# Kernel optimization log

Hardware: AMD Instinct MI355X
Metric: run time of the kernel (lower is better)

## Reference

```python
import jax, jax.numpy as jnp
import numpy as np

B, N, K, D = 4, 8192, 16, 128
G = D // 4  # spatial-encoding groups, 4 feature channels each ('a4')
BN_EPS = 1e-5


def setup_inputs() -> dict:
    key = jax.random.key(0)
    ks = jax.random.split(key, 8)
    x = jax.random.normal(ks[0], (B, N, D), jnp.float32)
    xyz = jax.random.uniform(ks[1], (B, N, 3), jnp.float32)
    knn = jax.random.randint(ks[2], (B, N, K), 0, N)
    proj_w = jax.random.normal(ks[3], (D, D), jnp.float32) * 0.02  # nn.Linear(in,out,bias=False) weight [out,in]
    coor = jax.random.normal(ks[4], (G * 3,), jnp.float32) * 0.5   # init_coor(out_dim//4).flatten()
    scale = jnp.full((G,), 0.1, jnp.float32)                        # zeros + 0.1
    bn_weight = jnp.ones((D,), jnp.float32)                          # init=1.0
    bn_bias = jnp.zeros((D,), jnp.float32)
    return dict(x=x, xyz=xyz, knn=knn, proj_w=proj_w, coor=coor,
                scale=scale, bn_weight=bn_weight, bn_bias=bn_bias)


def reference(x, xyz, knn, proj_w, coor, scale, bn_weight, bn_bias):
    Bb, Nn, _ = x.shape
    # 1) linear projection (no bias)
    h = jnp.einsum('bnc,dc->bnd', x, proj_w)  # [B,N,D]
    # 2) learned spatial position encoding weights: (4, G) = [cx,cy,cz,scale^2]
    w = jnp.concatenate([coor.reshape(-1, 3).T, (scale * scale)[None, :]], axis=0)
    # 3) KNN gathers
    bidx = jnp.arange(Bb)[:, None, None]
    xyz_n = xyz[bidx, knn]                      # [B,N,K,3]
    rel = xyz_n - xyz[:, :, None, :]            # relative coords
    f4 = jnp.concatenate([rel, jnp.sum(rel * rel, axis=-1, keepdims=True)], axis=-1)  # [B,N,K,4]
    e = jnp.einsum('bnkf,fg->bnkg', f4, w)      # [B,N,K,G] encoding per group
    hn = h[bidx, knn]                           # [B,N,K,D] neighbor features
    # 4) add encoding per group of 4 channels, max-aggregate over K neighbors
    g = hn.reshape(Bb, Nn, K, G, 4) + e[..., None]
    agg = jnp.max(g, axis=2).reshape(Bb, Nn, D)
    # 5) BatchNorm1d over B*N rows (training-mode batch stats, biased var)
    flat = agg.reshape(-1, D)
    mean = jnp.mean(flat, axis=0)
    var = jnp.mean(jnp.square(flat - mean), axis=0)
    y = (flat - mean) * jax.lax.rsqrt(var + BN_EPS) * bn_weight + bn_bias
    return y.reshape(Bb, Nn, D)
```

## Files before the change

### kernel.cpp

```cpp
#include <hip/hip_runtime.h>
#include <math.h>

#define BB 4
#define NN 8192
#define KK 16
#define DD 128
#define GG 32
#define NPTS (BB * NN)
#define GATHER_BLOCKS 2048
#define BN_EPS 1e-5f

__global__ void transpose_w(const float* __restrict__ w, float* __restrict__ wt) {
    int i = blockIdx.x * 256 + threadIdx.x;
    int d = i >> 7;
    int c = i & 127;
    wt[c * 128 + d] = w[d * 128 + c];
}

__global__ __launch_bounds__(256) void gemm_h(const float* __restrict__ x,
                                              const float* __restrict__ wt,
                                              float* __restrict__ h) {
    __shared__ float xs[64][128];
    const int block_row = blockIdx.x * 64;
    const int t = threadIdx.x;

    const float4* xg = reinterpret_cast<const float4*>(x + (size_t)block_row * 128);
    float4* xs4 = reinterpret_cast<float4*>(&xs[0][0]);
#pragma unroll
    for (int i = 0; i < 8; ++i) xs4[t + 256 * i] = xg[t + 256 * i];
    __syncthreads();

    const int ty = t >> 5;
    const int tx = t & 31;
    const int r0 = ty * 8;
    const int c0 = tx * 4;

    float acc[8][4];
#pragma unroll
    for (int r = 0; r < 8; ++r)
#pragma unroll
        for (int j = 0; j < 4; ++j) acc[r][j] = 0.f;

    for (int c4 = 0; c4 < 32; ++c4) {
        float4 wv[4];
#pragma unroll
        for (int j = 0; j < 4; ++j)
            wv[j] = *reinterpret_cast<const float4*>(wt + (size_t)(c4 * 4 + j) * 128 + c0);
#pragma unroll
        for (int r = 0; r < 8; ++r) {
            float4 xv = *reinterpret_cast<const float4*>(&xs[r0 + r][c4 * 4]);
            const float xc[4] = {xv.x, xv.y, xv.z, xv.w};
#pragma unroll
            for (int j = 0; j < 4; ++j) {
                acc[r][0] = fmaf(xc[j], wv[j].x, acc[r][0]);
                acc[r][1] = fmaf(xc[j], wv[j].y, acc[r][1]);
                acc[r][2] = fmaf(xc[j], wv[j].z, acc[r][2]);
                acc[r][3] = fmaf(xc[j], wv[j].w, acc[r][3]);
            }
        }
    }

#pragma unroll
    for (int r = 0; r < 8; ++r) {
        float4 o = make_float4(acc[r][0], acc[r][1], acc[r][2], acc[r][3]);
        *reinterpret_cast<float4*>(h + (size_t)(block_row + r0 + r) * 128 + c0) = o;
    }
}

__global__ __launch_bounds__(256) void gather_max(const float* __restrict__ h,
                                                  const float* __restrict__ xyz,
                                                  const int* __restrict__ knn,
                                                  const float* __restrict__ coor,
                                                  const float* __restrict__ scale,
                                                  float* __restrict__ out,
                                                  float* __restrict__ partials) {
    const int t = threadIdx.x;
    const int g = t & 31;
    const int sub = t >> 5;

    const float c0w = coor[g * 3 + 0];
    const float c1w = coor[g * 3 + 1];
    const float c2w = coor[g * 3 + 2];
    const float sg = scale[g];
    const float s2 = sg * sg;

    float lsum[4] = {0.f, 0.f, 0.f, 0.f};
    float lsq[4]  = {0.f, 0.f, 0.f, 0.f};

#pragma unroll
    for (int it = 0; it < 2; ++it) {
        const int p = blockIdx.x * 16 + it * 8 + sub;
        const int b = p >> 13;
        const float* ctr = xyz + (size_t)p * 3;
        const float cx = ctr[0], cy = ctr[1], cz = ctr[2];
        const int* kn = knn + (size_t)p * KK;

        float4 acc = make_float4(-INFINITY, -INFINITY, -INFINITY, -INFINITY);

#pragma unroll
        for (int k = 0; k < KK; ++k) {
            const int idx = kn[k];
            const int row = b * NN + idx;
            const float* nb = xyz + (size_t)row * 3;
            const float rx = nb[0] - cx;
            const float ry = nb[1] - cy;
            const float rz = nb[2] - cz;
            const float r2 = rx * rx + ry * ry + rz * rz;
            const float e = rx * c0w + ry * c1w + rz * c2w + r2 * s2;
            const float4 hv = *reinterpret_cast<const float4*>(h + (size_t)row * 128 + g * 4);
            acc.x = fmaxf(acc.x, hv.x + e);
            acc.y = fmaxf(acc.y, hv.y + e);
            acc.z = fmaxf(acc.z, hv.z + e);
            acc.w = fmaxf(acc.w, hv.w + e);
        }

        *reinterpret_cast<float4*>(out + (size_t)p * 128 + g * 4) = acc;

        lsum[0] += acc.x; lsum[1] += acc.y; lsum[2] += acc.z; lsum[3] += acc.w;
        lsq[0] += acc.x * acc.x; lsq[1] += acc.y * acc.y;
        lsq[2] += acc.z * acc.z; lsq[3] += acc.w * acc.w;
    }

    __shared__ float red[8][128];
#pragma unroll
    for (int j = 0; j < 4; ++j) red[sub][g * 4 + j] = lsum[j];
    __syncthreads();
    if (t < 128) {
        float s = 0.f;
#pragma unroll
        for (int s8 = 0; s8 < 8; ++s8) s += red[s8][t];
        partials[(size_t)t * GATHER_BLOCKS + blockIdx.x] = s;
    }
    __syncthreads();
#pragma unroll
    for (int j = 0; j < 4; ++j) red[sub][g * 4 + j] = lsq[j];
    __syncthreads();
    if (t < 128) {
        float q = 0.f;
#pragma unroll
        for (int s8 = 0; s8 < 8; ++s8) q += red[s8][t];
        partials[(size_t)(128 + t) * GATHER_BLOCKS + blockIdx.x] = q;
    }
}

__global__ __launch_bounds__(256) void bn_stats(const float* __restrict__ partials,
                                                const float* __restrict__ bnw,
                                                const float* __restrict__ bnb,
                                                float* __restrict__ stats) {
    const int ch = blockIdx.x;
    const int t = threadIdx.x;
    const float* ps = partials + (size_t)ch * GATHER_BLOCKS;
    const float* pq = partials + (size_t)(128 + ch) * GATHER_BLOCKS;
    float s = 0.f, q = 0.f;
    for (int i = t; i < GATHER_BLOCKS; i += 256) { s += ps[i]; q += pq[i]; }
    __shared__ float rs[256], rq[256];
    rs[t] = s; rq[t] = q;
    __syncthreads();
    for (int off = 128; off > 0; off >>= 1) {
        if (t < off) { rs[t] += rs[t + off]; rq[t] += rq[t + off]; }
        __syncthreads();
    }
    if (t == 0) {
        const float inv_n = 1.0f / (float)NPTS;
        const float mean = rs[0] * inv_n;
        const float var = rq[0] * inv_n - mean * mean;
        const float rstd = rsqrtf(var + BN_EPS);
        const float A = rstd * bnw[ch];
        stats[ch] = A;
        stats[128 + ch] = bnb[ch] - mean * A;
    }
}

__global__ __launch_bounds__(256) void bn_apply(float* __restrict__ out,
                                                const float* __restrict__ stats) {
    const int i = blockIdx.x * 256 + threadIdx.x;
    const int ch4 = i & 31;
    float4 v = reinterpret_cast<float4*>(out)[i];
    const float4 A = reinterpret_cast<const float4*>(stats)[ch4];
    const float4 C = reinterpret_cast<const float4*>(stats + 128)[ch4];
    v.x = fmaf(v.x, A.x, C.x);
    v.y = fmaf(v.y, A.y, C.y);
    v.z = fmaf(v.z, A.z, C.z);
    v.w = fmaf(v.w, A.w, C.w);
    reinterpret_cast<float4*>(out)[i] = v;
}

extern "C" void kernel_launch(void* const* d_in, const int* in_sizes, int n_in,
                              void* d_out, int out_size, void* d_ws, size_t ws_size,
                              hipStream_t stream) {
    const float* x      = (const float*)d_in[0];
    const float* xyz    = (const float*)d_in[1];
    const int*   knn    = (const int*)d_in[2];
    const float* proj_w = (const float*)d_in[3];
    const float* coor   = (const float*)d_in[4];
    const float* scale  = (const float*)d_in[5];
    const float* bnw    = (const float*)d_in[6];
    const float* bnb    = (const float*)d_in[7];
    float* out = (float*)d_out;

    char* ws = (char*)d_ws;
    float* h        = (float*)(ws);
    float* wt       = (float*)(ws + (size_t)NPTS * DD * 4);
    float* partials = (float*)(ws + (size_t)NPTS * DD * 4 + 65536);
    float* stats    = (float*)(ws + (size_t)NPTS * DD * 4 + 65536
                               + (size_t)2 * 128 * GATHER_BLOCKS * 4);

    transpose_w<<<64, 256, 0, stream>>>(proj_w, wt);
    gemm_h<<<NPTS / 64, 256, 0, stream>>>(x, wt, h);
    gather_max<<<GATHER_BLOCKS, 256, 0, stream>>>(h, xyz, knn, coor, scale, out, partials);
    bn_stats<<<128, 256, 0, stream>>>(partials, bnw, bnb, stats);
    bn_apply<<<(NPTS * DD / 4) / 256, 256, 0, stream>>>(out, stats);
}
```

Before: 69.50 us.

## Fuse gather-max, BN stats and BN apply into one persistent kernel with grid barriers

Merges the gather/max kernel, the BN statistics reduction and the BN apply pass into a single kernel of 1024 co-resident blocks. Two atomic grid barriers separate the three phases, and each thread keeps its aggregated values in registers so the output is written once, already normalized. This removes two kernel launches and a full read-modify-write of the output tensor. Blocks are also remapped so each XCD works on one batch half, which should improve L2 locality of the neighbor gathers. The cost is a spin-barrier whose correctness depends on all blocks being resident at once, plus an extra memset launch to clear the flags.

```diff
diff --git a/kernel.cpp b/kernel.cpp
--- a/kernel.cpp
+++ b/kernel.cpp
@@ -7,7 +7,8 @@
 #define DD 128
 #define GG 32
 #define NPTS (BB * NN)
-#define GATHER_BLOCKS 2048
+#define FBLOCKS 1024
+#define PTS_PER_BLOCK 32
 #define BN_EPS 1e-5f
 
 __global__ void transpose_w(const float* __restrict__ w, float* __restrict__ wt) {
@@ -67,16 +68,42 @@
     }
 }
 
-__global__ __launch_bounds__(256) void gather_max(const float* __restrict__ h,
-                                                  const float* __restrict__ xyz,
-                                                  const int* __restrict__ knn,
-                                                  const float* __restrict__ coor,
-                                                  const float* __restrict__ scale,
-                                                  float* __restrict__ out,
-                                                  float* __restrict__ partials) {
+__device__ __forceinline__ void grid_barrier(int* cnt, int* gen) {
+    __syncthreads();
+    if (threadIdx.x == 0) {
+        int prev = __hip_atomic_fetch_add(cnt, 1, __ATOMIC_ACQ_REL, __HIP_MEMORY_SCOPE_AGENT);
+        if (prev == FBLOCKS - 1) {
+            __hip_atomic_store(gen, 1, __ATOMIC_RELEASE, __HIP_MEMORY_SCOPE_AGENT);
+        } else {
+            while (__hip_atomic_load(gen, __ATOMIC_RELAXED, __HIP_MEMORY_SCOPE_AGENT) == 0) {
+                __builtin_amdgcn_s_sleep(8);
+            }
+            (void)__hip_atomic_load(gen, __ATOMIC_ACQUIRE, __HIP_MEMORY_SCOPE_AGENT);
+        }
+    }
+    __syncthreads();
+}
+
+__global__ __launch_bounds__(256, 4) void fused_gbn(const float* __restrict__ h,
+                                                    const float* __restrict__ xyz,
+                                                    const int* __restrict__ knn,
+                                                    const float* __restrict__ coor,
+                                                    const float* __restrict__ scale,
+                                                    const float* __restrict__ bnw,
+                                                    const float* __restrict__ bnb,
+                                                    float* __restrict__ out,
+                                                    float* __restrict__ partials,
+                                                    float* __restrict__ stats,
+                                                    int* __restrict__ flags) {
     const int t = threadIdx.x;
     const int g = t & 31;
     const int sub = t >> 5;
+
+    const int xcd = blockIdx.x & 7;
+    const int jj = blockIdx.x >> 3;
+    const int slot = ((xcd & 1) << 7) + jj;
+    const int b = xcd >> 1;
+    const int pbase = (b << 13) + (slot << 5);
 
     const float c0w = coor[g * 3 + 0];
     const float c1w = coor[g * 3 + 1];
@@ -86,11 +113,11 @@
 
     float lsum[4] = {0.f, 0.f, 0.f, 0.f};
     float lsq[4]  = {0.f, 0.f, 0.f, 0.f};
-
-#pragma unroll
-    for (int it = 0; it < 2; ++it) {
-        const int p = blockIdx.x * 16 + it * 8 + sub;
-        const int b = p >> 13;
+    float4 accv[4];
+
+#pragma unroll
+    for (int it = 0; it < 4; ++it) {
+        const int p = pbase + it * 8 + sub;
         const float* ctr = xyz + (size_t)p * 3;
         const float cx = ctr[0], cy = ctr[1], cz = ctr[2];
         const int* kn = knn + (size_t)p * KK;
@@ -100,7 +127,7 @@
 #pragma unroll
         for (int k = 0; k < KK; ++k) {
             const int idx = kn[k];
-            const int row = b * NN + idx;
+            const int row = (b << 13) + idx;
             const float* nb = xyz + (size_t)row * 3;
             const float rx = nb[0] - cx;
             const float ry = nb[1] - cy;
@@ -114,8 +141,7 @@
             acc.w = fmaxf(acc.w, hv.w + e);
         }
 
-        *reinterpret_cast<float4*>(out + (size_t)p * 128 + g * 4) = acc;
-
+        accv[it] = acc;
         lsum[0] += acc.x; lsum[1] += acc.y; lsum[2] += acc.z; lsum[3] += acc.w;
         lsq[0] += acc.x * acc.x; lsq[1] += acc.y * acc.y;
         lsq[2] += acc.z * acc.z; lsq[3] += acc.w * acc.w;
@@ -129,7 +155,7 @@
         float s = 0.f;
 #pragma unroll
         for (int s8 = 0; s8 < 8; ++s8) s += red[s8][t];
-        partials[(size_t)t * GATHER_BLOCKS + blockIdx.x] = s;
+        partials[(size_t)t * FBLOCKS + blockIdx.x] = s;
     }
     __syncthreads();
 #pragma unroll
@@ -139,50 +165,49 @@
         float q = 0.f;
 #pragma unroll
         for (int s8 = 0; s8 < 8; ++s8) q += red[s8][t];
-        partials[(size_t)(128 + t) * GATHER_BLOCKS + blockIdx.x] = q;
-    }
-}
-
-__global__ __launch_bounds__(256) void bn_stats(const float* __restrict__ partials,
-                                                const float* __restrict__ bnw,
-                                                const float* __restrict__ bnb,
-                                                float* __restrict__ stats) {
-    const int ch = blockIdx.x;
-    const int t = threadIdx.x;
-    const float* ps = partials + (size_t)ch * GATHER_BLOCKS;
-    const float* pq = partials + (size_t)(128 + ch) * GATHER_BLOCKS;
-    float s = 0.f, q = 0.f;
-    for (int i = t; i < GATHER_BLOCKS; i += 256) { s += ps[i]; q += pq[i]; }
-    __shared__ float rs[256], rq[256];
-    rs[t] = s; rq[t] = q;
-    __syncthreads();
-    for (int off = 128; off > 0; off >>= 1) {
-        if (t < off) { rs[t] += rs[t + off]; rq[t] += rq[t + off]; }
+        partials[(size_t)(128 + t) * FBLOCKS + blockIdx.x] = q;
+    }
+
+    grid_barrier(flags + 0, flags + 1);
+
+    if (blockIdx.x < 128) {
+        const int ch = blockIdx.x;
+        const float* ps = partials + (size_t)ch * FBLOCKS;
+        const float* pq = partials + (size_t)(128 + ch) * FBLOCKS;
+        float s = 0.f, q = 0.f;
+        for (int i = t; i < FBLOCKS; i += 256) { s += ps[i]; q += pq[i]; }
+        __shared__ float rs[256], rq[256];
+        rs[t] = s; rq[t] = q;
         __syncthreads();
-    }
-    if (t == 0) {
-        const float inv_n = 1.0f / (float)NPTS;
-        const float mean = rs[0] * inv_n;
-        const float var = rq[0] * inv_n - mean * mean;
-        const float rstd = rsqrtf(var + BN_EPS);
-        const float A = rstd * bnw[ch];
-        stats[ch] = A;
-        stats[128 + ch] = bnb[ch] - mean * A;
-    }
-}
-
-__global__ __launch_bounds__(256) void bn_apply(float* __restrict__ out,
-                                                const float* __restrict__ stats) {
-    const int i = blockIdx.x * 256 + threadIdx.x;
-    const int ch4 = i & 31;
-    float4 v = reinterpret_cast<float4*>(out)[i];
-    const float4 A = reinterpret_cast<const float4*>(stats)[ch4];
-    const float4 C = reinterpret_cast<const float4*>(stats + 128)[ch4];
-    v.x = fmaf(v.x, A.x, C.x);
-    v.y = fmaf(v.y, A.y, C.y);
-    v.z = fmaf(v.z, A.z, C.z);
-    v.w = fmaf(v.w, A.w, C.w);
-    reinterpret_cast<float4*>(out)[i] = v;
+        for (int off = 128; off > 0; off >>= 1) {
+            if (t < off) { rs[t] += rs[t + off]; rq[t] += rq[t + off]; }
+            __syncthreads();
+        }
+        if (t == 0) {
+            const float inv_n = 1.0f / (float)NPTS;
+            const float mean = rs[0] * inv_n;
+            const float var = rq[0] * inv_n - mean * mean;
+            const float rstd = rsqrtf(var + BN_EPS);
+            const float A = rstd * bnw[ch];
+            stats[ch] = A;
+            stats[128 + ch] = bnb[ch] - mean * A;
+        }
+    }
+
+    grid_barrier(flags + 2, flags + 3);
+
+    const float4 A = *reinterpret_cast<const float4*>(stats + g * 4);
+    const float4 C = *reinterpret_cast<const float4*>(stats + 128 + g * 4);
+#pragma unroll
+    for (int it = 0; it < 4; ++it) {
+        const int p = pbase + it * 8 + sub;
+        float4 v = accv[it];
+        v.x = fmaf(v.x, A.x, C.x);
+        v.y = fmaf(v.y, A.y, C.y);
+        v.z = fmaf(v.z, A.z, C.z);
+        v.w = fmaf(v.w, A.w, C.w);
+        *reinterpret_cast<float4*>(out + (size_t)p * 128 + g * 4) = v;
+    }
 }
 
 extern "C" void kernel_launch(void* const* d_in, const int* in_sizes, int n_in,
@@ -199,15 +224,16 @@
     float* out = (float*)d_out;
 
     char* ws = (char*)d_ws;
-    float* h        = (float*)(ws);
-    float* wt       = (float*)(ws + (size_t)NPTS * DD * 4);
-    float* partials = (float*)(ws + (size_t)NPTS * DD * 4 + 65536);
-    float* stats    = (float*)(ws + (size_t)NPTS * DD * 4 + 65536
-                               + (size_t)2 * 128 * GATHER_BLOCKS * 4);
-
+    size_t off = 0;
+    float* h        = (float*)(ws + off); off += (size_t)NPTS * DD * 4;
+    float* wt       = (float*)(ws + off); off += 65536;
+    float* partials = (float*)(ws + off); off += (size_t)2 * 128 * FBLOCKS * 4;
+    float* stats    = (float*)(ws + off); off += 1024;
+    int*   flags    = (int*)(ws + off);
+
+    hipMemsetAsync(flags, 0, 16, stream);
     transpose_w<<<64, 256, 0, stream>>>(proj_w, wt);
     gemm_h<<<NPTS / 64, 256, 0, stream>>>(x, wt, h);
-    gather_max<<<GATHER_BLOCKS, 256, 0, stream>>>(h, xyz, knn, coor, scale, out, partials);
-    bn_stats<<<128, 256, 0, stream>>>(partials, bnw, bnb, stats);
-    bn_apply<<<(NPTS * DD / 4) / 256, 256, 0, stream>>>(out, stats);
-}
+    fused_gbn<<<FBLOCKS, 256, 0, stream>>>(h, xyz, knn, coor, scale, bnw, bnb,
+                                           out, partials, stats, flags);
+}
```

New measurement: 231.7 us. 3.33x slower.
